# Kernel tuning notes

Hardware: AMD Instinct MI355X
Metric: run time of the kernel (lower is better)

The kernel has to match this reference:

```python
import jax, jax.numpy as jnp
import numpy as np

V = 128000  # vocab (input_size == output_size)
H = 2048    # hidden_size


def setup_inputs() -> dict:
    key = jax.random.key(0)
    ks = jax.random.split(key, 12)
    s = 0.02
    return {
        "input_tok": jax.random.randint(ks[0], (1,), 0, V),
        "h0": jnp.zeros((1, 1, H), jnp.float32),
        "c0": jnp.zeros((1, 1, H), jnp.float32),
        "emb": jax.random.normal(ks[1], (V, H), jnp.float32) * s,
        "W_ih": jax.random.normal(ks[2], (4 * H, H), jnp.float32) * s,
        "W_hh": jax.random.normal(ks[3], (4 * H, H), jnp.float32) * s,
        "b_ih": jnp.zeros((4 * H,), jnp.float32),
        "b_hh": jnp.zeros((4 * H,), jnp.float32),
        "W_attn": jax.random.normal(ks[4], (H, 2 * H), jnp.float32) * s,
        "b_attn": jnp.zeros((H,), jnp.float32),
        "v": jax.random.uniform(ks[5], (H,), jnp.float32),
        "W_out": jax.random.normal(ks[6], (V, 2 * H), jnp.float32) * s,
        "b_out": jnp.zeros((V,), jnp.float32),
    }


def reference(input_tok, h0, c0, emb, W_ih, W_hh, b_ih, b_hh,
              W_attn, b_attn, v, W_out, b_out):
    # --- embedding (single token, batch=1) ---
    x = emb[input_tok[0]]                      # [H]
    # --- single-layer, single-step LSTM (torch gate order i,f,g,o) ---
    gates = W_ih @ x + b_ih + W_hh @ h0[0, 0] + b_hh   # [4H]
    i, f, g, o = jnp.split(gates, 4)
    i, f, o = jax.nn.sigmoid(i), jax.nn.sigmoid(f), jax.nn.sigmoid(o)
    g = jnp.tanh(g)
    c1 = f * c0[0, 0] + i * g                  # [H]
    h1 = o * jnp.tanh(c1)                      # [H]

    output = h1[None, None, :]                 # [1,1,H] lstm output seq
    h_new = h1[None, None, :]                  # [L=1,1,H] (hidden[0])
    c_new = c1[None, None, :]

    # --- Bahdanau attention: query = output[-1], keys = hidden state ---
    q = output[-1]                             # [1,H]
    enc = jnp.transpose(h_new, (1, 0, 2))      # [1,L,H]
    L = enc.shape[1]
    q_rep = jnp.broadcast_to(q[:, None, :], (1, L, H))        # [1,L,H]
    energy = jnp.tanh(jnp.concatenate([q_rep, enc], axis=2) @ W_attn.T + b_attn)
    scores = jnp.einsum('blh,h->bl', energy, v)               # [1,L]
    attn_w = jax.nn.softmax(scores, axis=1)[:, None, :]       # [1,1,L]

    out_t = jnp.transpose(output, (1, 0, 2))                  # [1,1,H]
    context = jnp.einsum('bol,blh->boh', attn_w, out_t)[:, 0] # [1,H]

    # --- output projection on [output; context] + log_softmax ---
    feat = jnp.concatenate([output[0], context], axis=1)      # [1,2H]
    logits = feat @ W_out.T + b_out                           # [1,V]
    logp = jax.nn.log_softmax(logits, axis=1)
    return logp, (h_new, c_new), attn_w
```

## Files before the change

kernel.cpp:

```cpp
#include <hip/hip_runtime.h>
#include <math.h>

#define HH 2048
#define VV 128000

__device__ __forceinline__ float wave_sum(float v) {
    #pragma unroll
    for (int off = 32; off > 0; off >>= 1) v += __shfl_down(v, off, 64);
    return v;
}

__device__ __forceinline__ void lse_combine(float& m, float& s, float m2, float s2) {
    float mn = fmaxf(m, m2);
    s = s * expf(m - mn) + s2 * expf(m2 - mn);
    m = mn;
}

__global__ __launch_bounds__(256) void lstm_cell_kernel(
    const int* __restrict__ tok, const float* __restrict__ emb,
    const float* __restrict__ W_ih, const float* __restrict__ W_hh,
    const float* __restrict__ b_ih, const float* __restrict__ b_hh,
    const float* __restrict__ h0, const float* __restrict__ c0,
    float* __restrict__ out)
{
    const int k    = blockIdx.x;
    const int wave = threadIdx.x >> 6;
    const int lane = threadIdx.x & 63;
    const int row  = wave * HH + k;

    const float4* wi = (const float4*)(W_ih + (size_t)row * HH);
    const float4* wh = (const float4*)(W_hh + (size_t)row * HH);
    const float4* x4 = (const float4*)(emb + (size_t)tok[0] * HH);
    const float4* h4 = (const float4*)h0;

    float acc = 0.f;
    #pragma unroll
    for (int it = 0; it < HH / 4 / 64; ++it) {
        const int i = lane + it * 64;
        float4 a = wi[i], b = x4[i];
        acc = fmaf(a.x, b.x, fmaf(a.y, b.y, fmaf(a.z, b.z, fmaf(a.w, b.w, acc))));
        float4 c = wh[i], d = h4[i];
        acc = fmaf(c.x, d.x, fmaf(c.y, d.y, fmaf(c.z, d.z, fmaf(c.w, d.w, acc))));
    }
    acc = wave_sum(acc);

    __shared__ float g[4];
    if (lane == 0) g[wave] = acc + b_ih[row] + b_hh[row];
    __syncthreads();

    if (threadIdx.x == 0) {
        float gi = 1.f / (1.f + expf(-g[0]));
        float gf = 1.f / (1.f + expf(-g[1]));
        float gg = tanhf(g[2]);
        float go = 1.f / (1.f + expf(-g[3]));
        float c1 = gf * c0[k] + gi * gg;
        float h1 = go * tanhf(c1);
        out[VV + k]       = h1;
        out[VV + HH + k]  = c1;
        if (k == 0) out[VV + 2 * HH] = 1.0f;
    }
}

__global__ __launch_bounds__(256) void logits_kernel(
    const float* __restrict__ W_out, const float* __restrict__ b_out,
    const float* __restrict__ h1, float* __restrict__ logits)
{
    const int row  = blockIdx.x * 4 + (threadIdx.x >> 6);
    const int lane = threadIdx.x & 63;

    const float4* w  = (const float4*)(W_out + (size_t)row * (2 * HH));
    const float4* h4 = (const float4*)h1;

    float acc = 0.f;
    #pragma unroll
    for (int it = 0; it < HH / 4 / 64; ++it) {
        const int i = lane + it * 64;
        float4 a  = w[i];
        float4 b  = w[i + HH / 4];
        float4 hv = h4[i];
        acc = fmaf(a.x + b.x, hv.x,
              fmaf(a.y + b.y, hv.y,
              fmaf(a.z + b.z, hv.z,
              fmaf(a.w + b.w, hv.w, acc))));
    }
    acc = wave_sum(acc);
    if (lane == 0) logits[row] = acc + b_out[row];
}

__global__ __launch_bounds__(1024) void lse_partial_kernel(
    const float* __restrict__ logits, float* __restrict__ part)
{
    const int i = blockIdx.x * 1024 + threadIdx.x;
    float m = logits[i];
    float s = 1.f;
    #pragma unroll
    for (int off = 32; off > 0; off >>= 1) {
        float m2 = __shfl_down(m, off, 64);
        float s2 = __shfl_down(s, off, 64);
        lse_combine(m, s, m2, s2);
    }
    __shared__ float sm[16], ss[16];
    const int lane = threadIdx.x & 63, wave = threadIdx.x >> 6;
    if (lane == 0) { sm[wave] = m; ss[wave] = s; }
    __syncthreads();
    if (threadIdx.x == 0) {
        for (int w = 1; w < 16; ++w) lse_combine(m, s, sm[w], ss[w]);
        part[2 * blockIdx.x]     = m;
        part[2 * blockIdx.x + 1] = s;
    }
}

__global__ void lse_final_kernel(const float* __restrict__ part, float* __restrict__ lse)
{
    const int lane = threadIdx.x;
    float m = -INFINITY, s = 0.f;
    for (int i = lane; i < 125; i += 64)
        lse_combine(m, s, part[2 * i], part[2 * i + 1]);
    #pragma unroll
    for (int off = 32; off > 0; off >>= 1) {
        float m2 = __shfl_down(m, off, 64);
        float s2 = __shfl_down(s, off, 64);
        lse_combine(m, s, m2, s2);
    }
    if (lane == 0) lse[0] = m + logf(s);
}

__global__ __launch_bounds__(256) void logp_kernel(
    float* __restrict__ out, const float* __restrict__ lse)
{
    const int i = blockIdx.x * 256 + threadIdx.x;
    out[i] -= lse[0];
}

extern "C" void kernel_launch(void* const* d_in, const int* in_sizes, int n_in,
                              void* d_out, int out_size, void* d_ws, size_t ws_size,
                              hipStream_t stream) {
    const int*   tok    = (const int*)  d_in[0];
    const float* h0     = (const float*)d_in[1];
    const float* c0     = (const float*)d_in[2];
    const float* emb    = (const float*)d_in[3];
    const float* W_ih   = (const float*)d_in[4];
    const float* W_hh   = (const float*)d_in[5];
    const float* b_ih   = (const float*)d_in[6];
    const float* b_hh   = (const float*)d_in[7];
    const float* W_out  = (const float*)d_in[11];
    const float* b_out  = (const float*)d_in[12];

    float* out  = (float*)d_out;
    float* ws   = (float*)d_ws;
    float* lse  = ws;
    float* part = ws + 2;

    lstm_cell_kernel<<<HH, 256, 0, stream>>>(tok, emb, W_ih, W_hh, b_ih, b_hh, h0, c0, out);
    logits_kernel<<<VV / 4, 256, 0, stream>>>(W_out, b_out, out + VV, out);
    lse_partial_kernel<<<VV / 1024, 1024, 0, stream>>>(out, part);
    lse_final_kernel<<<1, 64, 0, stream>>>(part, lse);
    logp_kernel<<<VV / 256, 256, 0, stream>>>(out, lse);
}
```

Baseline: 372.8 us.

## Fuse logits with partial log-sum-exp and merge final LSE into normalize kernel

The logits GEMV now runs as 1000 persistent-style blocks of 128 rows each, with h1 staged in LDS, and folds an online max/sum reduction into the same kernel. The separate lse partial, final and logp kernels become one normalize kernel in which every block redundantly reduces the 1000 partials before subtracting. Weight streams use nontemporal loads to avoid polluting cache. This removes two launches and a reread of the logits, at the cost of fewer blocks for the bandwidth-bound GEMV and redundant partial reductions in each of the 500 normalize blocks.

```diff
diff --git a/kernel.cpp b/kernel.cpp
--- a/kernel.cpp
+++ b/kernel.cpp
@@ -3,6 +3,11 @@
 
 #define HH 2048
 #define VV 128000
+#define NB2 1000
+#define ROWS_PER_BLOCK 128
+#define TPB 256
+
+typedef float vf4 __attribute__((ext_vector_type(4)));
 
 __device__ __forceinline__ float wave_sum(float v) {
     #pragma unroll
@@ -14,6 +19,10 @@
     float mn = fmaxf(m, m2);
     s = s * expf(m - mn) + s2 * expf(m2 - mn);
     m = mn;
+}
+
+__device__ __forceinline__ vf4 ntload(const vf4* p) {
+    return __builtin_nontemporal_load(p);
 }
 
 __global__ __launch_bounds__(256) void lstm_cell_kernel(
@@ -28,18 +37,18 @@
     const int lane = threadIdx.x & 63;
     const int row  = wave * HH + k;
 
-    const float4* wi = (const float4*)(W_ih + (size_t)row * HH);
-    const float4* wh = (const float4*)(W_hh + (size_t)row * HH);
-    const float4* x4 = (const float4*)(emb + (size_t)tok[0] * HH);
-    const float4* h4 = (const float4*)h0;
+    const vf4* wi = (const vf4*)(W_ih + (size_t)row * HH);
+    const vf4* wh = (const vf4*)(W_hh + (size_t)row * HH);
+    const vf4* x4 = (const vf4*)(emb + (size_t)tok[0] * HH);
+    const vf4* h4 = (const vf4*)h0;
 
     float acc = 0.f;
     #pragma unroll
     for (int it = 0; it < HH / 4 / 64; ++it) {
         const int i = lane + it * 64;
-        float4 a = wi[i], b = x4[i];
+        vf4 a = ntload(&wi[i]), b = x4[i];
         acc = fmaf(a.x, b.x, fmaf(a.y, b.y, fmaf(a.z, b.z, fmaf(a.w, b.w, acc))));
-        float4 c = wh[i], d = h4[i];
+        vf4 c = ntload(&wh[i]), d = h4[i];
         acc = fmaf(c.x, d.x, fmaf(c.y, d.y, fmaf(c.z, d.z, fmaf(c.w, d.w, acc))));
     }
     acc = wave_sum(acc);
@@ -55,66 +64,74 @@
         float go = 1.f / (1.f + expf(-g[3]));
         float c1 = gf * c0[k] + gi * gg;
         float h1 = go * tanhf(c1);
-        out[VV + k]       = h1;
-        out[VV + HH + k]  = c1;
+        out[VV + k]      = h1;
+        out[VV + HH + k] = c1;
         if (k == 0) out[VV + 2 * HH] = 1.0f;
     }
 }
 
-__global__ __launch_bounds__(256) void logits_kernel(
+__global__ __launch_bounds__(TPB) void logits_lse_kernel(
     const float* __restrict__ W_out, const float* __restrict__ b_out,
-    const float* __restrict__ h1, float* __restrict__ logits)
+    const float* __restrict__ h1g, float* __restrict__ out,
+    float* __restrict__ part)
 {
-    const int row  = blockIdx.x * 4 + (threadIdx.x >> 6);
+    const int b    = blockIdx.x;
+    const int wave = threadIdx.x >> 6;
     const int lane = threadIdx.x & 63;
 
-    const float4* w  = (const float4*)(W_out + (size_t)row * (2 * HH));
-    const float4* h4 = (const float4*)h1;
+    __shared__ float h_lds[HH];
+    __shared__ float red_m[4], red_s[4];
 
-    float acc = 0.f;
-    #pragma unroll
-    for (int it = 0; it < HH / 4 / 64; ++it) {
-        const int i = lane + it * 64;
-        float4 a  = w[i];
-        float4 b  = w[i + HH / 4];
-        float4 hv = h4[i];
-        acc = fmaf(a.x + b.x, hv.x,
-              fmaf(a.y + b.y, hv.y,
-              fmaf(a.z + b.z, hv.z,
-              fmaf(a.w + b.w, hv.w, acc))));
+    for (int i = threadIdx.x; i < HH / 4; i += TPB)
+        ((vf4*)h_lds)[i] = ((const vf4*)h1g)[i];
+    __syncthreads();
+
+    const vf4* hl = (const vf4*)h_lds;
+    float m = -INFINITY, s = 0.f;
+
+    #pragma unroll 1
+    for (int j = 0; j < ROWS_PER_BLOCK / 4; ++j) {
+        const int row = b * ROWS_PER_BLOCK + j * 4 + wave;
+        const vf4* w = (const vf4*)(W_out + (size_t)row * (2 * HH));
+        float acc = 0.f;
+        #pragma unroll
+        for (int it = 0; it < HH / 4 / 64; ++it) {
+            const int i = lane + it * 64;
+            vf4 a  = ntload(&w[i]);
+            vf4 b2 = ntload(&w[i + HH / 4]);
+            vf4 hv = hl[i];
+            acc = fmaf(a.x + b2.x, hv.x,
+                  fmaf(a.y + b2.y, hv.y,
+                  fmaf(a.z + b2.z, hv.z,
+                  fmaf(a.w + b2.w, hv.w, acc))));
+        }
+        acc = wave_sum(acc);
+        if (lane == 0) {
+            const float lg = acc + b_out[row];
+            out[row] = lg;
+            lse_combine(m, s, lg, 1.f);
+        }
     }
-    acc = wave_sum(acc);
-    if (lane == 0) logits[row] = acc + b_out[row];
-}
-
-__global__ __launch_bounds__(1024) void lse_partial_kernel(
-    const float* __restrict__ logits, float* __restrict__ part)
-{
-    const int i = blockIdx.x * 1024 + threadIdx.x;
-    float m = logits[i];
-    float s = 1.f;
-    #pragma unroll
-    for (int off = 32; off > 0; off >>= 1) {
-        float m2 = __shfl_down(m, off, 64);
-        float s2 = __shfl_down(s, off, 64);
-        lse_combine(m, s, m2, s2);
-    }
-    __shared__ float sm[16], ss[16];
-    const int lane = threadIdx.x & 63, wave = threadIdx.x >> 6;
-    if (lane == 0) { sm[wave] = m; ss[wave] = s; }
+    if (lane == 0) { red_m[wave] = m; red_s[wave] = s; }
     __syncthreads();
     if (threadIdx.x == 0) {
-        for (int w = 1; w < 16; ++w) lse_combine(m, s, sm[w], ss[w]);
-        part[2 * blockIdx.x]     = m;
-        part[2 * blockIdx.x + 1] = s;
+        float bm = red_m[0], bs = red_s[0];
+        for (int w2 = 1; w2 < 4; ++w2) lse_combine(bm, bs, red_m[w2], red_s[w2]);
+        part[2 * b]     = bm;
+        part[2 * b + 1] = bs;
     }
 }
 
-__global__ void lse_final_kernel(const float* __restrict__ part, float* __restrict__ lse)
+__global__ __launch_bounds__(TPB) void lse_norm_kernel(
+    const float* __restrict__ part, float* __restrict__ out)
 {
-    const int lane = threadIdx.x;
+    const int wave = threadIdx.x >> 6;
+    const int lane = threadIdx.x & 63;
+    __shared__ float red_m[4], red_s[4];
+    __shared__ float lse_s;
+
     float m = -INFINITY, s = 0.f;
-    for (int i = lane; i < 125; i += 64)
+    for (int i = threadIdx.x; i < NB2; i += TPB)
         lse_combine(m, s, part[2 * i], part[2 * i + 1]);
     #pragma unroll
     for (int off = 32; off > 0; off >>= 1) {
@@ -122,14 +139,18 @@
         float s2 = __shfl_down(s, off, 64);
         lse_combine(m, s, m2, s2);
     }
-    if (lane == 0) lse[0] = m + logf(s);
-}
+    if (lane == 0) { red_m[wave] = m; red_s[wave] = s; }
+    __syncthreads();
+    if (threadIdx.x == 0) {
+        float bm = red_m[0], bs = red_s[0];
+        for (int w2 = 1; w2 < 4; ++w2) lse_combine(bm, bs, red_m[w2], red_s[w2]);
+        lse_s = bm + logf(bs);
+    }
+    __syncthreads();
 
-__global__ __launch_bounds__(256) void logp_kernel(
-    float* __restrict__ out, const float* __restrict__ lse)
-{
-    const int i = blockIdx.x * 256 + threadIdx.x;
-    out[i] -= lse[0];
+    const float lse = lse_s;
+    const int i = blockIdx.x * TPB + threadIdx.x;
+    out[i] -= lse;
 }
 
 extern "C" void kernel_launch(void* const* d_in, const int* in_sizes, int n_in,
@@ -147,13 +168,9 @@
     const float* b_out  = (const float*)d_in[12];
 
     float* out  = (float*)d_out;
-    float* ws   = (float*)d_ws;
-    float* lse  = ws;
-    float* part = ws + 2;
+    float* part = (float*)d_ws;
 
     lstm_cell_kernel<<<HH, 256, 0, stream>>>(tok, emb, W_ih, W_hh, b_ih, b_hh, h0, c0, out);
-    logits_kernel<<<VV / 4, 256, 0, stream>>>(W_out, b_out, out + VV, out);
-    lse_partial_kernel<<<VV / 1024, 1024, 0, stream>>>(out, part);
-    lse_final_kernel<<<1, 64, 0, stream>>>(part, lse);
-    logp_kernel<<<VV / 256, 256, 0, stream>>>(out, lse);
+    logits_lse_kernel<<<NB2, TPB, 0, stream>>>(W_out, b_out, out + VV, out, part);
+    lse_norm_kernel<<<VV / TPB, TPB, 0, stream>>>(part, out);
 }
```

Result: faster. 336.0 us (-9.9%).
